# Optimization experiments

Measured on AMD Instinct MI355X. Metric: run time of the kernel, lower is better.

The kernel has to match this reference:

```python
import jax, jax.numpy as jnp
import numpy as np

B, S, HID = 2, 2048, 4096
H, KH, D = 32, 8, 128
WINDOW = 1024
THETA = 1000000.0


def setup_inputs() -> dict:
    key = jax.random.key(0)
    ks = jax.random.split(key, 5)
    scale = 0.02
    hidden_states = jax.random.normal(ks[0], (B, S, HID), dtype=jnp.float32)
    wq = jax.random.normal(ks[1], (HID, H * D), dtype=jnp.float32) * scale
    wk = jax.random.normal(ks[2], (HID, KH * D), dtype=jnp.float32) * scale
    wv = jax.random.normal(ks[3], (HID, KH * D), dtype=jnp.float32) * scale
    wo = jax.random.normal(ks[4], (H * D, HID), dtype=jnp.float32) * scale
    position_ids = jnp.broadcast_to(jnp.arange(S, dtype=jnp.int64 if jax.config.jax_enable_x64 else jnp.int32), (B, S))
    return {"hidden_states": hidden_states, "position_ids": position_ids,
            "wq": wq, "wk": wk, "wv": wv, "wo": wo}


def _rope_sin_cos(position_ids):
    # inv_freq over even dims, emb = concat(freqs, freqs) -> [b, s, D]
    inv_freq = 1.0 / (THETA ** (jnp.arange(0, D, 2, dtype=jnp.float32) / D))
    angles = position_ids.astype(jnp.float32)[..., None] * inv_freq  # [b, s, D/2]
    emb = jnp.concatenate([angles, angles], axis=-1)  # [b, s, D]
    return jnp.sin(emb)[:, None, :, :], jnp.cos(emb)[:, None, :, :]  # [b,1,s,D]


def _rotate_half(x):
    x1, x2 = jnp.split(x, 2, axis=-1)
    return jnp.concatenate([-x2, x1], axis=-1)


def _apply_rope(x, sin, cos):
    return x * cos + _rotate_half(x) * sin


def reference(hidden_states, position_ids, wq, wk, wv, wo):
    b, s, _ = hidden_states.shape
    # projections -> [b, heads, s, d]
    q = (hidden_states @ wq).reshape(b, s, H, D).transpose(0, 2, 1, 3)
    k = (hidden_states @ wk).reshape(b, s, KH, D).transpose(0, 2, 1, 3)
    v = (hidden_states @ wv).reshape(b, s, KH, D).transpose(0, 2, 1, 3)
    sin, cos = _rope_sin_cos(position_ids)
    q = _apply_rope(q, sin, cos)
    k = _apply_rope(k, sin, cos)
    # repeat kv heads for GQA: [b, KH, s, d] -> [b, H, s, d]
    rep = H // KH
    k = jnp.repeat(k, rep, axis=1)
    v = jnp.repeat(v, rep, axis=1)
    # sliding-window causal mask
    i = jnp.arange(s)[:, None]
    j = jnp.arange(s)[None, :]
    mask = (j <= i) & (i - j < WINDOW)  # [s, s]
    scores = jnp.einsum("bhqd,bhkd->bhqk", q, k) / jnp.sqrt(jnp.asarray(D, q.dtype))
    neg = jnp.finfo(scores.dtype).min
    scores = jnp.where(mask[None, None, :, :], scores, neg)
    attn = jax.nn.softmax(scores, axis=-1)
    out = jnp.einsum("bhqk,bhkd->bhqd", attn, v)
    out = out.transpose(0, 2, 1, 3).reshape(b, s, H * D)
    return out @ wo
```

## Files before the change

### kernel.cpp

```cpp
#include <hip/hip_runtime.h>
#include <hip/hip_bf16.h>
#include <math.h>

typedef __attribute__((ext_vector_type(8))) __bf16 bf16x8;
typedef __attribute__((ext_vector_type(4))) float f32x4;

#define MFMA16(a, b, c) __builtin_amdgcn_mfma_f32_16x16x32_bf16((a), (b), (c), 0, 0, 0)

__device__ inline void gld_lds16(const __hip_bfloat16* g, __hip_bfloat16* l) {
    __builtin_amdgcn_global_load_lds(
        (const __attribute__((address_space(1))) void*)g,
        (__attribute__((address_space(3))) void*)l, 16, 0, 0);
}

__global__ void cast_bf16_kernel(const float* __restrict__ in, __hip_bfloat16* __restrict__ out) {
    int i = (blockIdx.x * blockDim.x + threadIdx.x) * 4;
    float4 v = *(const float4*)(in + i);
    out[i + 0] = __float2bfloat16(v.x);
    out[i + 1] = __float2bfloat16(v.y);
    out[i + 2] = __float2bfloat16(v.z);
    out[i + 3] = __float2bfloat16(v.w);
}

__global__ void transpose_cast_kernel(const float* __restrict__ w, __hip_bfloat16* __restrict__ wt,
                                      int K, int N) {
    __shared__ float tile[32][33];
    int n0 = blockIdx.x * 32, k0 = blockIdx.y * 32;
    int tx = threadIdx.x;
    int ty = threadIdx.y;
#pragma unroll
    for (int r = 0; r < 4; r++) {
        int k = k0 + ty + r * 8;
        tile[ty + r * 8][tx] = w[(size_t)k * N + n0 + tx];
    }
    __syncthreads();
#pragma unroll
    for (int r = 0; r < 4; r++) {
        int n = n0 + ty + r * 8;
        wt[(size_t)n * K + k0 + tx] = __float2bfloat16(tile[tx][ty + r * 8]);
    }
}

__global__ __launch_bounds__(256) void gemm_qkv_kernel(
    const __hip_bfloat16* __restrict__ Xb,
    const __hip_bfloat16* __restrict__ Wt,
    __hip_bfloat16* __restrict__ Qraw,
    __hip_bfloat16* __restrict__ Kraw,
    __hip_bfloat16* __restrict__ Vtt) {
    const int K = 4096;
    __shared__ __hip_bfloat16 As[128 * 32];
    __shared__ __hip_bfloat16 Bs[128 * 32];

    int tid = threadIdx.x;
    int wave = tid >> 6, lane = tid & 63;
    int l15 = lane & 15, quad = lane >> 4;
    int m0 = blockIdx.y * 128, n0 = blockIdx.x * 128;

    int srow = wave * 32 + (lane >> 2);
    int scol = (lane & 3) * 8;
    const __hip_bfloat16* agp0 = Xb + (size_t)(m0 + srow) * K + scol;
    const __hip_bfloat16* agp1 = agp0 + (size_t)16 * K;
    const __hip_bfloat16* bgp0 = Wt + (size_t)(n0 + srow) * K + scol;
    const __hip_bfloat16* bgp1 = bgp0 + (size_t)16 * K;
    __hip_bfloat16* asl0 = As + wave * 1024;
    __hip_bfloat16* asl1 = asl0 + 512;
    __hip_bfloat16* bsl0 = Bs + wave * 1024;
    __hip_bfloat16* bsl1 = bsl0 + 512;

    int wm = wave & 1, wn = wave >> 1;
    const __hip_bfloat16* afr = As + (size_t)(wm * 64 + l15) * 32 + quad * 8;
    const __hip_bfloat16* bfr = Bs + (size_t)(wn * 64 + l15) * 32 + quad * 8;

    f32x4 acc[4][4];
#pragma unroll
    for (int mi = 0; mi < 4; mi++)
#pragma unroll
        for (int ni = 0; ni < 4; ni++) acc[mi][ni] = (f32x4){0.f, 0.f, 0.f, 0.f};

    for (int k0 = 0; k0 < K; k0 += 32) {
        gld_lds16(agp0 + k0, asl0);
        gld_lds16(agp1 + k0, asl1);
        gld_lds16(bgp0 + k0, bsl0);
        gld_lds16(bgp1 + k0, bsl1);
        __syncthreads();
        bf16x8 a[4], b[4];
#pragma unroll
        for (int mi = 0; mi < 4; mi++) a[mi] = *(const bf16x8*)(afr + mi * 16 * 32);
#pragma unroll
        for (int ni = 0; ni < 4; ni++) b[ni] = *(const bf16x8*)(bfr + ni * 16 * 32);
#pragma unroll
        for (int mi = 0; mi < 4; mi++)
#pragma unroll
            for (int ni = 0; ni < 4; ni++) acc[mi][ni] = MFMA16(a[mi], b[ni], acc[mi][ni]);
        __syncthreads();
    }

#pragma unroll
    for (int mi = 0; mi < 4; mi++) {
#pragma unroll
        for (int ni = 0; ni < 4; ni++) {
            int n = n0 + wn * 64 + ni * 16 + l15;
#pragma unroll
            for (int r = 0; r < 4; r++) {
                int m = m0 + wm * 64 + mi * 16 + quad * 4 + r;
                int bb = m >> 11, s = m & 2047;
                __hip_bfloat16 hv = __float2bfloat16(acc[mi][ni][r]);
                if (n < 4096) {
                    int hh = n >> 7, d = n & 127;
                    Qraw[(((size_t)(bb * 32 + hh)) * 2048 + s) * 128 + d] = hv;
                } else if (n < 5120) {
                    int n2 = n - 4096, hh = n2 >> 7, d = n2 & 127;
                    Kraw[(((size_t)(bb * 8 + hh)) * 2048 + s) * 128 + d] = hv;
                } else {
                    int n2 = n - 5120, hh = n2 >> 7, d = n2 & 127;
                    Vtt[((((size_t)(bb * 8 + hh)) * 32 + (s >> 6)) * 128 + d) * 64 + (s & 63)] = hv;
                }
            }
        }
    }
}

__global__ __launch_bounds__(256) void gemm_out_kernel(
    const __hip_bfloat16* __restrict__ A, const __hip_bfloat16* __restrict__ Bt,
    float* __restrict__ C) {
    const int K = 4096, N = 4096;
    __shared__ __hip_bfloat16 As[128 * 32];
    __shared__ __hip_bfloat16 Bs[128 * 32];

    int tid = threadIdx.x;
    int wave = tid >> 6, lane = tid & 63;
    int l15 = lane & 15, quad = lane >> 4;
    int m0 = blockIdx.y * 128, n0 = blockIdx.x * 128;

    int srow = wave * 32 + (lane >> 2);
    int scol = (lane & 3) * 8;
    const __hip_bfloat16* agp0 = A + (size_t)(m0 + srow) * K + scol;
    const __hip_bfloat16* agp1 = agp0 + (size_t)16 * K;
    const __hip_bfloat16* bgp0 = Bt + (size_t)(n0 + srow) * K + scol;
    const __hip_bfloat16* bgp1 = bgp0 + (size_t)16 * K;
    __hip_bfloat16* asl0 = As + wave * 1024;
    __hip_bfloat16* asl1 = asl0 + 512;
    __hip_bfloat16* bsl0 = Bs + wave * 1024;
    __hip_bfloat16* bsl1 = bsl0 + 512;

    int wm = wave & 1, wn = wave >> 1;
    const __hip_bfloat16* afr = As + (size_t)(wm * 64 + l15) * 32 + quad * 8;
    const __hip_bfloat16* bfr = Bs + (size_t)(wn * 64 + l15) * 32 + quad * 8;

    f32x4 acc[4][4];
#pragma unroll
    for (int mi = 0; mi < 4; mi++)
#pragma unroll
        for (int ni = 0; ni < 4; ni++) acc[mi][ni] = (f32x4){0.f, 0.f, 0.f, 0.f};

    for (int k0 = 0; k0 < K; k0 += 32) {
        gld_lds16(agp0 + k0, asl0);
        gld_lds16(agp1 + k0, asl1);
        gld_lds16(bgp0 + k0, bsl0);
        gld_lds16(bgp1 + k0, bsl1);
        __syncthreads();
        bf16x8 a[4], b[4];
#pragma unroll
        for (int mi = 0; mi < 4; mi++) a[mi] = *(const bf16x8*)(afr + mi * 16 * 32);
#pragma unroll
        for (int ni = 0; ni < 4; ni++) b[ni] = *(const bf16x8*)(bfr + ni * 16 * 32);
#pragma unroll
        for (int mi = 0; mi < 4; mi++)
#pragma unroll
            for (int ni = 0; ni < 4; ni++) acc[mi][ni] = MFMA16(a[mi], b[ni], acc[mi][ni]);
        __syncthreads();
    }

#pragma unroll
    for (int mi = 0; mi < 4; mi++) {
#pragma unroll
        for (int ni = 0; ni < 4; ni++) {
            int n = n0 + wn * 64 + ni * 16 + l15;
#pragma unroll
            for (int r = 0; r < 4; r++) {
                int m = m0 + wm * 64 + mi * 16 + quad * 4 + r;
                C[(size_t)m * N + n] = acc[mi][ni][r];
            }
        }
    }
}

__global__ void rope_kernel(__hip_bfloat16* __restrict__ x, const int* __restrict__ pos_ids,
                            int nheads) {
    int idx = blockIdx.x * blockDim.x + threadIdx.x;
    int d = idx & 63;
    int s = (idx >> 6) & 2047;
    int bh = idx >> 17;
    int b = bh / nheads;
    float p = (float)pos_ids[b * 2048 + s];
    float inv = exp2f(-(float)d * 0.31143075889f);
    float ang = p * inv;
    float sn, cs;
    __sincosf(ang, &sn, &cs);
    size_t base = ((size_t)bh * 2048 + s) * 128;
    float x1 = __bfloat162float(x[base + d]);
    float x2 = __bfloat162float(x[base + d + 64]);
    x[base + d]      = __float2bfloat16(x1 * cs - x2 * sn);
    x[base + d + 64] = __float2bfloat16(x2 * cs + x1 * sn);
}

__global__ __launch_bounds__(256) void attn_kernel(
    const __hip_bfloat16* __restrict__ Qb, const __hip_bfloat16* __restrict__ Kb,
    const __hip_bfloat16* __restrict__ Vtt, __hip_bfloat16* __restrict__ AO) {
    const int S = 2048, D = 128;
    __shared__ __hip_bfloat16 Ks[64 * 128];
    __shared__ __hip_bfloat16 Vs[128 * 64];
    __shared__ __hip_bfloat16 Pl[4][16][72];

    int tid = threadIdx.x;
    int wave = tid >> 6, lane = tid & 63;
    int l15 = lane & 15, quad = lane >> 4;
    int base = blockIdx.x * 64;
    int i0 = base + wave * 16;
    int h = blockIdx.y, b = blockIdx.z;
    int kh = h >> 2;
    const __hip_bfloat16* Qh = Qb + (size_t)(b * 32 + h) * S * D;
    const __hip_bfloat16* Kh = Kb + (size_t)(b * 8 + kh) * S * D;
    const __hip_bfloat16* Vh = Vtt + (size_t)(b * 8 + kh) * S * D;

    bf16x8 qf[4];
    {
        const __hip_bfloat16* qrow = Qh + (size_t)(i0 + l15) * D + quad * 8;
#pragma unroll
        for (int kk = 0; kk < 4; kk++) qf[kk] = *(const bf16x8*)(qrow + kk * 32);
    }
    f32x4 o[8];
#pragma unroll
    for (int f = 0; f < 8; f++) o[f] = (f32x4){0.f, 0.f, 0.f, 0.f};
    float lrow[4] = {0.f, 0.f, 0.f, 0.f};

    int kst = (base > 1023) ? ((base - 1023) & ~63) : 0;
    const float c2 = 0.12751878882f;
    int e3 = l15 & 7;

    for (int key0 = kst; key0 <= base; key0 += 64) {
#pragma unroll
        for (int i = 0; i < 4; i++) {
            int rb = wave * 16 + i * 4;
            int row = rb + (lane >> 4);
            int c = (lane & 15) ^ (row & 7);
            gld_lds16(Kh + (size_t)(key0 + row) * 128 + c * 8, Ks + rb * 128);
        }
        const __hip_bfloat16* Vtile = Vh + (size_t)(key0 >> 6) * (128 * 64);
#pragma unroll
        for (int i = 0; i < 4; i++) {
            int db = wave * 32 + i * 8;
            int row = db + (lane >> 3);
            int c = (lane & 7) ^ (row & 7);
            gld_lds16(Vtile + (size_t)row * 64 + c * 8, Vs + db * 64);
        }
        __syncthreads();

        bool alive = (key0 <= i0 + 15) && (key0 + 63 >= i0 - 1023);
        if (alive) {
            f32x4 sc[4];
#pragma unroll
            for (int kb = 0; kb < 4; kb++) {
                sc[kb] = (f32x4){0.f, 0.f, 0.f, 0.f};
                const __hip_bfloat16* krow = Ks + (kb * 16 + l15) * 128;
#pragma unroll
                for (int kk = 0; kk < 4; kk++) {
                    int slot = ((kk << 2) | quad) ^ e3;
                    bf16x8 kf = *(const bf16x8*)(krow + slot * 8);
                    sc[kb] = MFMA16(qf[kk], kf, sc[kb]);
                }
            }
            bool interior = (key0 + 63 <= i0) && (key0 >= i0 - 1008);
            if (interior) {
#pragma unroll
                for (int kb = 0; kb < 4; kb++)
#pragma unroll
                    for (int r = 0; r < 4; r++) {
                        float p = __builtin_amdgcn_exp2f(sc[kb][r] * c2);
                        lrow[r] += p;
                        Pl[wave][quad * 4 + r][kb * 16 + l15] = __float2bfloat16(p);
                    }
            } else {
#pragma unroll
                for (int kb = 0; kb < 4; kb++)
#pragma unroll
                    for (int r = 0; r < 4; r++) {
                        int i = i0 + quad * 4 + r;
                        int j = key0 + kb * 16 + l15;
                        float v = (j <= i && i - j < 1024) ? sc[kb][r] * c2 : -1e30f;
                        float p = __builtin_amdgcn_exp2f(v);
                        lrow[r] += p;
                        Pl[wave][quad * 4 + r][kb * 16 + l15] = __float2bfloat16(p);
                    }
            }
            bf16x8 pf0 = *(const bf16x8*)(&Pl[wave][l15][quad * 8]);
            bf16x8 pf1 = *(const bf16x8*)(&Pl[wave][l15][32 + quad * 8]);
            int s0 = quad ^ e3, s1 = (4 + quad) ^ e3;
#pragma unroll
            for (int f = 0; f < 8; f++) {
                const __hip_bfloat16* vrow = Vs + (f * 16 + l15) * 64;
                bf16x8 v0 = *(const bf16x8*)(vrow + s0 * 8);
                bf16x8 v1 = *(const bf16x8*)(vrow + s1 * 8);
                o[f] = MFMA16(pf0, v0, o[f]);
                o[f] = MFMA16(pf1, v1, o[f]);
            }
        }
        __syncthreads();
    }

#pragma unroll
    for (int r = 0; r < 4; r++) {
#pragma unroll
        for (int msk = 1; msk < 16; msk <<= 1) lrow[r] += __shfl_xor(lrow[r], msk, 64);
    }
#pragma unroll
    for (int r = 0; r < 4; r++) {
        int srow = i0 + quad * 4 + r;
        float invl = 1.f / lrow[r];
        __hip_bfloat16* orow = AO + ((size_t)(b * 2048 + srow) * 4096) + h * 128;
#pragma unroll
        for (int f = 0; f < 8; f++) orow[f * 16 + l15] = __float2bfloat16(o[f][r] * invl);
    }
}

extern "C" void kernel_launch(void* const* d_in, const int* in_sizes, int n_in,
                              void* d_out, int out_size, void* d_ws, size_t ws_size,
                              hipStream_t stream) {
    (void)in_sizes; (void)n_in; (void)out_size;
    const float* hidden = (const float*)d_in[0];
    const int* pos = (const int*)d_in[1];
    const float* wq = (const float*)d_in[2];
    const float* wk = (const float*)d_in[3];
    const float* wv = (const float*)d_in[4];
    const float* wo = (const float*)d_in[5];
    float* out = (float*)d_out;

    const int M = 4096;
    char* ws = (char*)d_ws;
    size_t off = 0;
    auto alloc = [&](size_t bytes) { char* p = ws + off; off += bytes; return p; };
    __hip_bfloat16* Xb    = (__hip_bfloat16*)alloc((size_t)M * 4096 * 2);
    __hip_bfloat16* Wqkvt = (__hip_bfloat16*)alloc((size_t)6144 * 4096 * 2);
    __hip_bfloat16* Wot   = (__hip_bfloat16*)alloc((size_t)4096 * 4096 * 2);
    __hip_bfloat16* Qb    = (__hip_bfloat16*)alloc((size_t)M * 4096 * 2);
    __hip_bfloat16* Kb    = (__hip_bfloat16*)alloc((size_t)M * 1024 * 2);
    __hip_bfloat16* Vtt   = (__hip_bfloat16*)alloc((size_t)M * 1024 * 2);
    __hip_bfloat16* AO    = (__hip_bfloat16*)alloc((size_t)M * 4096 * 2);
    if (off > ws_size) return;

    cast_bf16_kernel<<<(M * 4096) / 1024, 256, 0, stream>>>(hidden, Xb);
    dim3 tb(32, 8);
    transpose_cast_kernel<<<dim3(128, 128), tb, 0, stream>>>(wq, Wqkvt, 4096, 4096);
    transpose_cast_kernel<<<dim3(32, 128),  tb, 0, stream>>>(wk, Wqkvt + (size_t)4096 * 4096, 4096, 1024);
    transpose_cast_kernel<<<dim3(32, 128),  tb, 0, stream>>>(wv, Wqkvt + (size_t)5120 * 4096, 4096, 1024);
    transpose_cast_kernel<<<dim3(128, 128), tb, 0, stream>>>(wo, Wot, 4096, 4096);

    gemm_qkv_kernel<<<dim3(48, 32), 256, 0, stream>>>(Xb, Wqkvt, Qb, Kb, Vtt);

    rope_kernel<<<(2 * 32 * 2048 * 64) / 256, 256, 0, stream>>>(Qb, pos, 32);
    rope_kernel<<<(2 * 8 * 2048 * 64) / 256, 256, 0, stream>>>(Kb, pos, 8);

    attn_kernel<<<dim3(32, 32, 2), 256, 0, stream>>>(Qb, Kb, Vtt, AO);

    gemm_out_kernel<<<dim3(32, 32), 256, 0, stream>>>(AO, Wot, out);
}
```

Measured before the change: 811.3 us.

## Share GEMM core with BK=64 tiles and XOR-swizzled LDS layout

Both projection GEMMs now use one templated 128x128 core that loads 64-wide K slices per iteration instead of 32, halving the number of barrier pairs per K sweep. The LDS tile is stored with an XOR swizzle on 16-byte chunks so the fragment reads avoid bank conflicts. Each block now uses twice the shared memory, which may lower occupancy, and the loop still has no double buffering.

```diff
diff --git a/kernel.cpp b/kernel.cpp
--- a/kernel.cpp
+++ b/kernel.cpp
@@ -41,148 +41,127 @@
     }
 }
 
+struct GemmAcc {
+    f32x4 acc[4][4];
+};
+
+template <typename EPILOGUE>
+__device__ __forceinline__ void gemm128_bk64(
+    const __hip_bfloat16* __restrict__ A, const __hip_bfloat16* __restrict__ Bt,
+    int m0, int n0, int K, __hip_bfloat16* As, __hip_bfloat16* Bs, EPILOGUE epi) {
+    int tid = threadIdx.x;
+    int wave = tid >> 6, lane = tid & 63;
+    int l15 = lane & 15, quad = lane >> 4;
+
+    int lr = lane >> 3;
+    int c8 = (lane & 7) ^ lr;
+    const __hip_bfloat16* aG = A + (size_t)(m0 + wave * 8 + lr) * K + c8 * 8;
+    const __hip_bfloat16* bG = Bt + (size_t)(n0 + wave * 8 + lr) * K + c8 * 8;
+    __hip_bfloat16* aL = As + wave * 512;
+    __hip_bfloat16* bL = Bs + wave * 512;
+
+    int wm = wave & 1, wn = wave >> 1;
+    int e3 = l15 & 7;
+    int s0 = (quad ^ e3) * 8;
+    int s1 = ((4 + quad) ^ e3) * 8;
+    const __hip_bfloat16* afr = As + (wm * 64 + l15) * 64;
+    const __hip_bfloat16* bfr = Bs + (wn * 64 + l15) * 64;
+
+    f32x4 acc[4][4];
+#pragma unroll
+    for (int mi = 0; mi < 4; mi++)
+#pragma unroll
+        for (int ni = 0; ni < 4; ni++) acc[mi][ni] = (f32x4){0.f, 0.f, 0.f, 0.f};
+
+    for (int k0 = 0; k0 < K; k0 += 64) {
+#pragma unroll
+        for (int i = 0; i < 4; i++) {
+            gld_lds16(aG + k0 + (size_t)(i * 32) * K, aL + i * 2048);
+            gld_lds16(bG + k0 + (size_t)(i * 32) * K, bL + i * 2048);
+        }
+        __syncthreads();
+        bf16x8 a0[4], b0[4], a1[4], b1[4];
+#pragma unroll
+        for (int mi = 0; mi < 4; mi++) {
+            a0[mi] = *(const bf16x8*)(afr + mi * 1024 + s0);
+            a1[mi] = *(const bf16x8*)(afr + mi * 1024 + s1);
+        }
+#pragma unroll
+        for (int ni = 0; ni < 4; ni++) {
+            b0[ni] = *(const bf16x8*)(bfr + ni * 1024 + s0);
+            b1[ni] = *(const bf16x8*)(bfr + ni * 1024 + s1);
+        }
+#pragma unroll
+        for (int mi = 0; mi < 4; mi++)
+#pragma unroll
+            for (int ni = 0; ni < 4; ni++) {
+                acc[mi][ni] = MFMA16(a0[mi], b0[ni], acc[mi][ni]);
+                acc[mi][ni] = MFMA16(a1[mi], b1[ni], acc[mi][ni]);
+            }
+        __syncthreads();
+    }
+    epi(acc, wm, wn, l15, quad);
+}
+
 __global__ __launch_bounds__(256) void gemm_qkv_kernel(
     const __hip_bfloat16* __restrict__ Xb,
     const __hip_bfloat16* __restrict__ Wt,
     __hip_bfloat16* __restrict__ Qraw,
     __hip_bfloat16* __restrict__ Kraw,
     __hip_bfloat16* __restrict__ Vtt) {
-    const int K = 4096;
-    __shared__ __hip_bfloat16 As[128 * 32];
-    __shared__ __hip_bfloat16 Bs[128 * 32];
-
-    int tid = threadIdx.x;
-    int wave = tid >> 6, lane = tid & 63;
-    int l15 = lane & 15, quad = lane >> 4;
+    __shared__ __hip_bfloat16 As[128 * 64];
+    __shared__ __hip_bfloat16 Bs[128 * 64];
     int m0 = blockIdx.y * 128, n0 = blockIdx.x * 128;
-
-    int srow = wave * 32 + (lane >> 2);
-    int scol = (lane & 3) * 8;
-    const __hip_bfloat16* agp0 = Xb + (size_t)(m0 + srow) * K + scol;
-    const __hip_bfloat16* agp1 = agp0 + (size_t)16 * K;
-    const __hip_bfloat16* bgp0 = Wt + (size_t)(n0 + srow) * K + scol;
-    const __hip_bfloat16* bgp1 = bgp0 + (size_t)16 * K;
-    __hip_bfloat16* asl0 = As + wave * 1024;
-    __hip_bfloat16* asl1 = asl0 + 512;
-    __hip_bfloat16* bsl0 = Bs + wave * 1024;
-    __hip_bfloat16* bsl1 = bsl0 + 512;
-
-    int wm = wave & 1, wn = wave >> 1;
-    const __hip_bfloat16* afr = As + (size_t)(wm * 64 + l15) * 32 + quad * 8;
-    const __hip_bfloat16* bfr = Bs + (size_t)(wn * 64 + l15) * 32 + quad * 8;
-
-    f32x4 acc[4][4];
-#pragma unroll
-    for (int mi = 0; mi < 4; mi++)
-#pragma unroll
-        for (int ni = 0; ni < 4; ni++) acc[mi][ni] = (f32x4){0.f, 0.f, 0.f, 0.f};
-
-    for (int k0 = 0; k0 < K; k0 += 32) {
-        gld_lds16(agp0 + k0, asl0);
-        gld_lds16(agp1 + k0, asl1);
-        gld_lds16(bgp0 + k0, bsl0);
-        gld_lds16(bgp1 + k0, bsl1);
-        __syncthreads();
-        bf16x8 a[4], b[4];
-#pragma unroll
-        for (int mi = 0; mi < 4; mi++) a[mi] = *(const bf16x8*)(afr + mi * 16 * 32);
-#pragma unroll
-        for (int ni = 0; ni < 4; ni++) b[ni] = *(const bf16x8*)(bfr + ni * 16 * 32);
-#pragma unroll
-        for (int mi = 0; mi < 4; mi++)
-#pragma unroll
-            for (int ni = 0; ni < 4; ni++) acc[mi][ni] = MFMA16(a[mi], b[ni], acc[mi][ni]);
-        __syncthreads();
-    }
-
-#pragma unroll
-    for (int mi = 0; mi < 4; mi++) {
-#pragma unroll
-        for (int ni = 0; ni < 4; ni++) {
-            int n = n0 + wn * 64 + ni * 16 + l15;
-#pragma unroll
-            for (int r = 0; r < 4; r++) {
-                int m = m0 + wm * 64 + mi * 16 + quad * 4 + r;
-                int bb = m >> 11, s = m & 2047;
-                __hip_bfloat16 hv = __float2bfloat16(acc[mi][ni][r]);
-                if (n < 4096) {
-                    int hh = n >> 7, d = n & 127;
-                    Qraw[(((size_t)(bb * 32 + hh)) * 2048 + s) * 128 + d] = hv;
-                } else if (n < 5120) {
-                    int n2 = n - 4096, hh = n2 >> 7, d = n2 & 127;
-                    Kraw[(((size_t)(bb * 8 + hh)) * 2048 + s) * 128 + d] = hv;
-                } else {
-                    int n2 = n - 5120, hh = n2 >> 7, d = n2 & 127;
-                    Vtt[((((size_t)(bb * 8 + hh)) * 32 + (s >> 6)) * 128 + d) * 64 + (s & 63)] = hv;
+    gemm128_bk64(Xb, Wt, m0, n0, 4096, As, Bs,
+        [&](f32x4 (&acc)[4][4], int wm, int wn, int l15, int quad) {
+#pragma unroll
+            for (int mi = 0; mi < 4; mi++) {
+#pragma unroll
+                for (int ni = 0; ni < 4; ni++) {
+                    int n = n0 + wn * 64 + ni * 16 + l15;
+#pragma unroll
+                    for (int r = 0; r < 4; r++) {
+                        int m = m0 + wm * 64 + mi * 16 + quad * 4 + r;
+                        int bb = m >> 11, s = m & 2047;
+                        __hip_bfloat16 hv = __float2bfloat16(acc[mi][ni][r]);
+                        if (n < 4096) {
+                            int hh = n >> 7, d = n & 127;
+                            Qraw[(((size_t)(bb * 32 + hh)) * 2048 + s) * 128 + d] = hv;
+                        } else if (n < 5120) {
+                            int n2 = n - 4096, hh = n2 >> 7, d = n2 & 127;
+                            Kraw[(((size_t)(bb * 8 + hh)) * 2048 + s) * 128 + d] = hv;
+                        } else {
+                            int n2 = n - 5120, hh = n2 >> 7, d = n2 & 127;
+                            Vtt[((((size_t)(bb * 8 + hh)) * 32 + (s >> 6)) * 128 + d) * 64 + (s & 63)] = hv;
+                        }
+                    }
                 }
             }
-        }
-    }
+        });
 }
 
 __global__ __launch_bounds__(256) void gemm_out_kernel(
     const __hip_bfloat16* __restrict__ A, const __hip_bfloat16* __restrict__ Bt,
     float* __restrict__ C) {
-    const int K = 4096, N = 4096;
-    __shared__ __hip_bfloat16 As[128 * 32];
-    __shared__ __hip_bfloat16 Bs[128 * 32];
-
-    int tid = threadIdx.x;
-    int wave = tid >> 6, lane = tid & 63;
-    int l15 = lane & 15, quad = lane >> 4;
+    __shared__ __hip_bfloat16 As[128 * 64];
+    __shared__ __hip_bfloat16 Bs[128 * 64];
     int m0 = blockIdx.y * 128, n0 = blockIdx.x * 128;
-
-    int srow = wave * 32 + (lane >> 2);
-    int scol = (lane & 3) * 8;
-    const __hip_bfloat16* agp0 = A + (size_t)(m0 + srow) * K + scol;
-    const __hip_bfloat16* agp1 = agp0 + (size_t)16 * K;
-    const __hip_bfloat16* bgp0 = Bt + (size_t)(n0 + srow) * K + scol;
-    const __hip_bfloat16* bgp1 = bgp0 + (size_t)16 * K;
-    __hip_bfloat16* asl0 = As + wave * 1024;
-    __hip_bfloat16* asl1 = asl0 + 512;
-    __hip_bfloat16* bsl0 = Bs + wave * 1024;
-    __hip_bfloat16* bsl1 = bsl0 + 512;
-
-    int wm = wave & 1, wn = wave >> 1;
-    const __hip_bfloat16* afr = As + (size_t)(wm * 64 + l15) * 32 + quad * 8;
-    const __hip_bfloat16* bfr = Bs + (size_t)(wn * 64 + l15) * 32 + quad * 8;
-
-    f32x4 acc[4][4];
-#pragma unroll
-    for (int mi = 0; mi < 4; mi++)
-#pragma unroll
-        for (int ni = 0; ni < 4; ni++) acc[mi][ni] = (f32x4){0.f, 0.f, 0.f, 0.f};
-
-    for (int k0 = 0; k0 < K; k0 += 32) {
-        gld_lds16(agp0 + k0, asl0);
-        gld_lds16(agp1 + k0, asl1);
-        gld_lds16(bgp0 + k0, bsl0);
-        gld_lds16(bgp1 + k0, bsl1);
-        __syncthreads();
-        bf16x8 a[4], b[4];
-#pragma unroll
-        for (int mi = 0; mi < 4; mi++) a[mi] = *(const bf16x8*)(afr + mi * 16 * 32);
-#pragma unroll
-        for (int ni = 0; ni < 4; ni++) b[ni] = *(const bf16x8*)(bfr + ni * 16 * 32);
-#pragma unroll
-        for (int mi = 0; mi < 4; mi++)
-#pragma unroll
-            for (int ni = 0; ni < 4; ni++) acc[mi][ni] = MFMA16(a[mi], b[ni], acc[mi][ni]);
-        __syncthreads();
-    }
-
-#pragma unroll
-    for (int mi = 0; mi < 4; mi++) {
-#pragma unroll
-        for (int ni = 0; ni < 4; ni++) {
-            int n = n0 + wn * 64 + ni * 16 + l15;
-#pragma unroll
-            for (int r = 0; r < 4; r++) {
-                int m = m0 + wm * 64 + mi * 16 + quad * 4 + r;
-                C[(size_t)m * N + n] = acc[mi][ni][r];
-            }
-        }
-    }
+    gemm128_bk64(A, Bt, m0, n0, 4096, As, Bs,
+        [&](f32x4 (&acc)[4][4], int wm, int wn, int l15, int quad) {
+            const int N = 4096;
+#pragma unroll
+            for (int mi = 0; mi < 4; mi++) {
+#pragma unroll
+                for (int ni = 0; ni < 4; ni++) {
+                    int n = n0 + wn * 64 + ni * 16 + l15;
+#pragma unroll
+                    for (int r = 0; r < 4; r++) {
+                        int m = m0 + wm * 64 + mi * 16 + quad * 4 + r;
+                        C[(size_t)m * N + n] = acc[mi][ni][r];
+                    }
+                }
+            }
+        });
 }
 
 __global__ void rope_kernel(__hip_bfloat16* __restrict__ x, const int* __restrict__ pos_ids,
```

New measurement: 791.0 us. -2.5%, faster.
